# Kernel tuning notes

Measured on AMD Instinct MI355X. Metric: run time of the kernel, lower is better.

The kernel has to match this reference:

```python
import jax, jax.numpy as jnp
import numpy as np

B, S, D = 1, 1024, 1024
NH, NKV, HD = 16, 4, 64
E, K, HE = 64, 6, 512
EPS = 1e-5


def rmsnorm(x, w, eps=EPS):
    return w * (x * jax.lax.rsqrt(jnp.mean(x * x, axis=-1, keepdims=True) + eps))


def rope(x, cos, sin):
    # x: [b, s, h, hd]; cos/sin: [s, hd//2]; pairs are consecutive elements
    x2 = x.reshape(*x.shape[:-1], -1, 2)
    x0, x1 = x2[..., 0], x2[..., 1]
    c = cos[None, :, None, :]
    s = sin[None, :, None, :]
    o0 = x0 * c - x1 * s
    o1 = x0 * s + x1 * c
    return jnp.stack([o0, o1], axis=-1).reshape(x.shape)


def swiglu(x, w1, w3, w2):
    return (jax.nn.silu(x @ w1) * (x @ w3)) @ w2


def setup_inputs() -> dict:
    key = jax.random.key(0)
    ks = jax.random.split(key, 12)

    def w(k, shape, fan_in):
        return jax.random.normal(k, shape, jnp.float32) / np.sqrt(fan_in).astype(np.float32)

    # RoPE tables (theta = 10000), shape [S, HD//2]
    inv = 1.0 / (10000.0 ** (np.arange(0, HD, 2, dtype=np.float32) / HD))
    ang = np.arange(S, dtype=np.float32)[:, None] * inv[None, :]
    return {
        "x": jax.random.normal(ks[0], (B, S, D), jnp.float32),
        "freqs_cos": jnp.asarray(np.cos(ang), jnp.float32),
        "freqs_sin": jnp.asarray(np.sin(ang), jnp.float32),
        "attn_norm_w": jnp.ones((D,), jnp.float32),
        "ffn_norm_w": jnp.ones((D,), jnp.float32),
        "wq": w(ks[1], (D, NH * HD), D),
        "wk": w(ks[2], (D, NKV * HD), D),
        "wv": w(ks[3], (D, NKV * HD), D),
        "wo": w(ks[4], (NH * HD, D), NH * HD),
        "q_norm_w": jnp.ones((HD,), jnp.float32),
        "k_norm_w": jnp.ones((HD,), jnp.float32),
        "gate_w": w(ks[5], (D, E), D),
        "w1_e": w(ks[6], (E, D, HE), D),
        "w3_e": w(ks[7], (E, D, HE), D),
        "w2_e": w(ks[8], (E, HE, D), HE),
        "sw1": w(ks[9], (D, HE), D),
        "sw3": w(ks[10], (D, HE), D),
        "sw2": w(ks[11], (HE, D), HE),
    }


def reference(x, freqs_cos, freqs_sin, attn_norm_w, ffn_norm_w, wq, wk, wv, wo,
              q_norm_w, k_norm_w, gate_w, w1_e, w3_e, w2_e, sw1, sw3, sw2):
    b, s, d = x.shape
    # ---- attention (GQA + RoPE, causal) ----
    hx = rmsnorm(x, attn_norm_w)
    q = (hx @ wq).reshape(b, s, NH, HD)
    k = (hx @ wk).reshape(b, s, NKV, HD)
    v = (hx @ wv).reshape(b, s, NKV, HD)
    q = rmsnorm(q, q_norm_w)
    k = rmsnorm(k, k_norm_w)
    q = rope(q, freqs_cos, freqs_sin)
    k = rope(k, freqs_cos, freqs_sin)
    n_rep = NH // NKV
    k = jnp.repeat(k, n_rep, axis=2)  # [b,s,NH,HD]
    v = jnp.repeat(v, n_rep, axis=2)
    scores = jnp.einsum("bqhd,bkhd->bhqk", q, k) / jnp.float32(np.sqrt(HD))
    causal = jnp.tril(jnp.ones((s, s), bool))
    scores = jnp.where(causal[None, None], scores, jnp.finfo(scores.dtype).min)
    attn = jax.nn.softmax(scores, axis=-1)
    o = jnp.einsum("bhqk,bkhd->bqhd", attn, v).reshape(b, s, NH * HD) @ wo
    h = x + o

    # ---- MoE SwiGLU (top-k routing, renormalized) ----
    z = rmsnorm(h, ffn_norm_w).reshape(-1, d)  # [T, D]
    T = z.shape[0]
    probs = jax.nn.softmax(z @ gate_w, axis=-1)  # [T, E]
    topw, sel = jax.lax.top_k(probs, K)
    topw = topw / jnp.sum(topw, axis=-1, keepdims=True)
    # dense combine matrix C[t,e] = routing weight (0 if not selected)
    C = jnp.zeros((T, E), z.dtype).at[jnp.arange(T)[:, None], sel].add(topw)
    # expert SwiGLU, combine weights applied before the down-projection
    h1 = jnp.einsum("td,edh->teh", z, w1_e)
    h3 = jnp.einsum("td,edh->teh", z, w3_e)
    g = (jax.nn.silu(h1) * h3) * C[:, :, None]
    moe_out = jnp.einsum("teh,ehd->td", g, w2_e)
    shared = swiglu(z, sw1, sw3, sw2)
    return h + (moe_out + shared).reshape(b, s, d)
```

## Files before the change

### kernel.cpp

```cpp
#include <hip/hip_runtime.h>
#include <hip/hip_bf16.h>
#include <math.h>

#define D_MODEL 1024
#define SEQ     1024
#define NHEADS  16
#define NKVH    4
#define HDIM    64
#define NEXP    64
#define TOPK    6
#define HEXP    512
#define EPS     1e-5f
#define MAXTILES 120

typedef __attribute__((ext_vector_type(8))) short bf16x8;
typedef __attribute__((ext_vector_type(4))) float f32x4;

struct bfrag2 { bf16x8 hi, lo; };
struct f32x8r { float v[8]; };

__device__ __forceinline__ unsigned rne1(float a) {
  union { float f; unsigned u; } x; x.f = a;
  return (x.u + 0x7fffu + ((x.u >> 16) & 1u)) >> 16;
}
__device__ __forceinline__ float frombf(unsigned h) {
  union { float f; unsigned u; } x; x.u = h << 16; return x.f;
}
__device__ __forceinline__ void split_pack(float a, float b, unsigned& hi, unsigned& lo) {
  unsigned ha = rne1(a), hb = rne1(b);
  hi = ha | (hb << 16);
  lo = rne1(a - frombf(ha)) | (rne1(b - frombf(hb)) << 16);
}
__device__ __forceinline__ unsigned pk2bf(float a, float b) {
  return rne1(a) | (rne1(b) << 16);
}

__device__ __forceinline__ f32x4 mfma16(bf16x8 a, bf16x8 b, f32x4 c) {
  return __builtin_amdgcn_mfma_f32_16x16x32_bf16(a, b, c, 0, 0, 0);
}
__device__ __forceinline__ f32x4 mfma_sp(bf16x8 ah, bf16x8 al, const bfrag2& b, f32x4 c) {
  c = mfma16(ah, b.hi, c);
  c = mfma16(ah, b.lo, c);
  c = mfma16(al, b.hi, c);
  return c;
}

__device__ __forceinline__ f32x8r loadraw8(const float* __restrict__ p, int ld) {
  f32x8r r;
#pragma unroll
  for (int i = 0; i < 8; i++) r.v[i] = p[(size_t)ld * i];
  return r;
}
__device__ __forceinline__ bf16x8 cvt_bf(const f32x8r& f) {
  union { bf16x8 v; unsigned u[4]; } r;
  r.u[0] = pk2bf(f.v[0], f.v[1]); r.u[1] = pk2bf(f.v[2], f.v[3]);
  r.u[2] = pk2bf(f.v[4], f.v[5]); r.u[3] = pk2bf(f.v[6], f.v[7]);
  return r.v;
}
__device__ __forceinline__ bfrag2 cvt_bf2(const f32x8r& f) {
  union { bf16x8 v; unsigned u[4]; } H, L;
  split_pack(f.v[0], f.v[1], H.u[0], L.u[0]);
  split_pack(f.v[2], f.v[3], H.u[1], L.u[1]);
  split_pack(f.v[4], f.v[5], H.u[2], L.u[2]);
  split_pack(f.v[6], f.v[7], H.u[3], L.u[3]);
  bfrag2 r; r.hi = H.v; r.lo = L.v; return r;
}

__global__ __launch_bounds__(256) void rmsnorm_k(const float* __restrict__ x,
    const float* __restrict__ w, float* __restrict__ out, ushort* __restrict__ outb) {
  int t = blockIdx.x;
  const float4* xr = (const float4*)(x + (size_t)t * D_MODEL);
  float4 v = xr[threadIdx.x];
  float ss = v.x*v.x + v.y*v.y + v.z*v.z + v.w*v.w;
  for (int off = 32; off; off >>= 1) ss += __shfl_xor(ss, off);
  __shared__ float red[4];
  if ((threadIdx.x & 63) == 0) red[threadIdx.x >> 6] = ss;
  __syncthreads();
  float tot = red[0] + red[1] + red[2] + red[3];
  float inv = rsqrtf(tot * (1.f / D_MODEL) + EPS);
  float4 wv = ((const float4*)w)[threadIdx.x];
  float4 o;
  o.x = v.x * inv * wv.x; o.y = v.y * inv * wv.y;
  o.z = v.z * inv * wv.z; o.w = v.w * inv * wv.w;
  ((float4*)(out + (size_t)t * D_MODEL))[threadIdx.x] = o;
  if (outb) {
    uint2 b;
    b.x = pk2bf(o.x, o.y); b.y = pk2bf(o.z, o.w);
    *(uint2*)(outb + (size_t)t * D_MODEL + threadIdx.x * 4) = b;
  }
}

__global__ __launch_bounds__(256) void mfma_gemm_k(const float* __restrict__ A,
    const float* __restrict__ B, float* __restrict__ C, float* __restrict__ C2,
    const float* __restrict__ resid, int N, int K) {
  __shared__ short Ah[2][16][40];
  __shared__ short Al[2][16][40];
  int bm = blockIdx.y << 4, bn = blockIdx.x << 7;
  int tid = threadIdx.x, wv = tid >> 6, lane = tid & 63;
  int m_ = tid >> 4, k_ = (tid & 15) << 1;
  int arow = lane & 15, akb = (lane >> 4) << 3;
  int c0 = bn + wv * 32 + arow;
  const float* ar = A + (size_t)(bm + m_) * K + k_;
  {
    float2 a0 = *(const float2*)ar;
    unsigned hi, lo; split_pack(a0.x, a0.y, hi, lo);
    *(unsigned*)&Ah[0][m_][k_] = hi;
    *(unsigned*)&Al[0][m_][k_] = lo;
  }
  float2 aO = *(const float2*)(ar + 32);
  float2 aE;
  f32x8r bE0 = loadraw8(B + (size_t)akb * N + c0, N);
  f32x8r bE1 = loadraw8(B + (size_t)akb * N + c0 + 16, N);
  f32x8r bO0 = loadraw8(B + (size_t)(32 + akb) * N + c0, N);
  f32x8r bO1 = loadraw8(B + (size_t)(32 + akb) * N + c0 + 16, N);
  __syncthreads();
  f32x4 acc0 = {0.f,0.f,0.f,0.f}, acc1 = {0.f,0.f,0.f,0.f};
  for (int k0 = 0; k0 < K; k0 += 64) {
    {
      int kp = (k0 + 64 < K) ? k0 + 64 : 0;
      f32x8r n0 = loadraw8(B + (size_t)(kp + akb) * N + c0, N);
      f32x8r n1 = loadraw8(B + (size_t)(kp + akb) * N + c0 + 16, N);
      float2 an = *(const float2*)(ar + kp);
      bfrag2 f0 = cvt_bf2(bE0), f1 = cvt_bf2(bE1);
      bf16x8 ah = *(const bf16x8*)&Ah[0][arow][akb];
      bf16x8 al = *(const bf16x8*)&Al[0][arow][akb];
      acc0 = mfma_sp(ah, al, f0, acc0);
      acc1 = mfma_sp(ah, al, f1, acc1);
      unsigned hi, lo; split_pack(aO.x, aO.y, hi, lo);
      *(unsigned*)&Ah[1][m_][k_] = hi;
      *(unsigned*)&Al[1][m_][k_] = lo;
      __syncthreads();
      bE0 = n0; bE1 = n1; aE = an;
    }
    {
      int kp = (k0 + 96 < K) ? k0 + 96 : 0;
      f32x8r n0 = loadraw8(B + (size_t)(kp + akb) * N + c0, N);
      f32x8r n1 = loadraw8(B + (size_t)(kp + akb) * N + c0 + 16, N);
      float2 an = *(const float2*)(ar + kp);
      bfrag2 f0 = cvt_bf2(bO0), f1 = cvt_bf2(bO1);
      bf16x8 ah = *(const bf16x8*)&Ah[1][arow][akb];
      bf16x8 al = *(const bf16x8*)&Al[1][arow][akb];
      acc0 = mfma_sp(ah, al, f0, acc0);
      acc1 = mfma_sp(ah, al, f1, acc1);
      unsigned hi, lo; split_pack(aE.x, aE.y, hi, lo);
      *(unsigned*)&Ah[0][m_][k_] = hi;
      *(unsigned*)&Al[0][m_][k_] = lo;
      __syncthreads();
      bO0 = n0; bO1 = n1; aO = an;
    }
  }
  int r0 = (lane >> 4) << 2;
#pragma unroll
  for (int ri = 0; ri < 4; ri++) {
    int row = bm + r0 + ri;
    size_t o0 = (size_t)row * N + c0;
    float v0 = acc0[ri], v1 = acc1[ri];
    if (resid) { v0 += resid[o0]; v1 += resid[o0 + 16]; }
    C[o0] = v0; C[o0 + 16] = v1;
    if (C2) { C2[o0] = v0; C2[o0 + 16] = v1; }
  }
}

__global__ __launch_bounds__(64) void qknorm_rope_k(float* __restrict__ qb,
    float* __restrict__ kb, const float* __restrict__ qw, const float* __restrict__ kw,
    const float* __restrict__ fcos, const float* __restrict__ fsin) {
  int t = blockIdx.x, hid = blockIdx.y, lane = threadIdx.x;
  float* p; const float* w;
  if (hid < NHEADS) { p = qb + (size_t)t * (NHEADS*HDIM) + hid * HDIM; w = qw; }
  else              { p = kb + (size_t)t * (NKVH*HDIM) + (hid - NHEADS) * HDIM; w = kw; }
  float v = p[lane];
  float ss = v * v;
  for (int off = 32; off; off >>= 1) ss += __shfl_xor(ss, off);
  float vn = v * rsqrtf(ss * (1.f / HDIM) + EPS) * w[lane];
  int pi = lane >> 1;
  float c = fcos[t * (HDIM/2) + pi], s = fsin[t * (HDIM/2) + pi];
  float other = __shfl_xor(vn, 1);
  float o = (lane & 1) ? (other * s + vn * c) : (vn * c - other * s);
  p[lane] = o;
}

__global__ __launch_bounds__(256) void attn_mfma(const float* __restrict__ qb,
    const float* __restrict__ kb, const float* __restrict__ vb, float* __restrict__ ob) {
  int h = blockIdx.y;
  int qbase = blockIdx.x << 6;
  int kvh = h >> 2;
  int tid = threadIdx.x, wv = tid >> 6, lane = tid & 63;
  __shared__ short Kt[64][72];
  __shared__ short Vt[64][72];
  __shared__ short Pl[4][16][72];
  int arow = lane & 15;
  int akb = (lane >> 4) << 3;
  int kg = lane >> 4;
  int qrow_base = qbase + wv * 16;
  bf16x8 qf[2];
  {
    const float* qp = qb + (size_t)(qrow_base + arow) * (NHEADS*HDIM) + h * HDIM;
#pragma unroll
    for (int c = 0; c < 2; c++) {
      int d0 = akb + c * 32;
      union { bf16x8 v; unsigned u[4]; } r;
#pragma unroll
      for (int j = 0; j < 4; j++) r.u[j] = pk2bf(qp[d0 + 2*j], qp[d0 + 2*j + 1]);
      qf[c] = r.v;
    }
  }
  f32x4 accO[4];
  float m_[4], l_[4];
#pragma unroll
  for (int n = 0; n < 4; n++) { accO[n] = (f32x4){0.f,0.f,0.f,0.f}; m_[n] = -1e30f; l_[n] = 0.f; }
  int ntiles = (qbase >> 6) + 1;
  for (int ti = 0; ti < ntiles; ti++) {
    int ts = ti << 6;
#pragma unroll
    for (int i = 0; i < 16; i++) {
      int flat = tid + i * 256;
      int kk = flat >> 6, dd = flat & 63;
      size_t src = (size_t)(ts + kk) * (NKVH*HDIM) + kvh * HDIM + dd;
      Kt[kk][dd] = (short)rne1(kb[src]);
      Vt[dd][kk] = (short)rne1(vb[src]);
    }
    __syncthreads();
    f32x4 accS[4];
#pragma unroll
    for (int n = 0; n < 4; n++) accS[n] = (f32x4){0.f,0.f,0.f,0.f};
#pragma unroll
    for (int c = 0; c < 2; c++) {
#pragma unroll
      for (int n = 0; n < 4; n++) {
        bf16x8 bf = *(const bf16x8*)&Kt[n*16 + arow][c*32 + akb];
        accS[n] = mfma16(qf[c], bf, accS[n]);
      }
    }
#pragma unroll
    for (int ri = 0; ri < 4; ri++) {
      int qrow = qrow_base + kg*4 + ri;
      float mx = -1e30f;
#pragma unroll
      for (int n = 0; n < 4; n++) {
        int key = ts + n*16 + arow;
        float s = (key <= qrow) ? accS[n][ri] * 0.125f : -1e30f;
        accS[n][ri] = s;
        mx = fmaxf(mx, s);
      }
      for (int off = 1; off < 16; off <<= 1) mx = fmaxf(mx, __shfl_xor(mx, off));
      float mn = fmaxf(m_[ri], mx);
      float a = __expf(m_[ri] - mn);
      float sum = 0.f;
#pragma unroll
      for (int n = 0; n < 4; n++) {
        float p = __expf(accS[n][ri] - mn);
        accS[n][ri] = p;
        sum += p;
      }
      for (int off = 1; off < 16; off <<= 1) sum += __shfl_xor(sum, off);
      l_[ri] = l_[ri] * a + sum;
      m_[ri] = mn;
#pragma unroll
      for (int n = 0; n < 4; n++) accO[n][ri] *= a;
    }
#pragma unroll
    for (int ri = 0; ri < 4; ri++)
#pragma unroll
      for (int n = 0; n < 4; n++)
        Pl[wv][kg*4 + ri][n*16 + arow] = (short)rne1(accS[n][ri]);
#pragma unroll
    for (int c = 0; c < 2; c++) {
      bf16x8 pf = *(const bf16x8*)&Pl[wv][arow][c*32 + akb];
#pragma unroll
      for (int n = 0; n < 4; n++) {
        bf16x8 vf = *(const bf16x8*)&Vt[n*16 + arow][c*32 + akb];
        accO[n] = mfma16(pf, vf, accO[n]);
      }
    }
    __syncthreads();
  }
#pragma unroll
  for (int ri = 0; ri < 4; ri++) {
    int qrow = qrow_base + kg*4 + ri;
    float inv = 1.f / l_[ri];
#pragma unroll
    for (int n = 0; n < 4; n++)
      ob[(size_t)qrow * (NHEADS*HDIM) + h * HDIM + n*16 + arow] = accO[n][ri] * inv;
  }
}

__global__ __launch_bounds__(64) void gate_topk_k(const float* __restrict__ z,
    const float* __restrict__ gw, int* __restrict__ sel, float* __restrict__ topw,
    int* __restrict__ counts) {
  int t = blockIdx.x, lane = threadIdx.x;
  const float* zr = z + (size_t)t * D_MODEL;
  float acc = 0.f;
  for (int d = 0; d < D_MODEL; d += 4) {
    float4 zv = *(const float4*)(zr + d);
    acc += zv.x * gw[(size_t)(d + 0) * NEXP + lane];
    acc += zv.y * gw[(size_t)(d + 1) * NEXP + lane];
    acc += zv.z * gw[(size_t)(d + 2) * NEXP + lane];
    acc += zv.w * gw[(size_t)(d + 3) * NEXP + lane];
  }
  float m = acc;
  for (int off = 32; off; off >>= 1) m = fmaxf(m, __shfl_xor(m, off));
  float p = __expf(acc - m);
  float s = p;
  for (int off = 32; off; off >>= 1) s += __shfl_xor(s, off);
  p /= s;
  float rem = p, wsum = 0.f;
  float wvv[TOPK]; int wi[TOPK];
  for (int i = 0; i < TOPK; i++) {
    float v = rem; int idx = lane;
    for (int off = 32; off; off >>= 1) {
      float v2 = __shfl_xor(v, off);
      int i2 = __shfl_xor(idx, off);
      if (v2 > v || (v2 == v && i2 < idx)) { v = v2; idx = i2; }
    }
    wvv[i] = v; wi[i] = idx; wsum += v;
    if (lane == idx) rem = -1.f;
  }
  if (lane < TOPK) {
    sel[t * TOPK + lane] = wi[lane];
    topw[t * TOPK + lane] = wvv[lane] / wsum;
  }
  if (lane == 0)
    for (int i = 0; i < TOPK; i++) atomicAdd(&counts[wi[i]], 1);
}

__global__ void scan_k(const int* __restrict__ counts, int* __restrict__ offs,
                       int* __restrict__ cursor, int* __restrict__ tile2e,
                       int* __restrict__ tile2mt, int* __restrict__ ntiles) {
  int lane = threadIdx.x;
  int c = counts[lane];
  int x = c;
  for (int off = 1; off < 64; off <<= 1) {
    int y = __shfl_up(x, off);
    if (lane >= off) x += y;
  }
  offs[lane] = x - c;
  cursor[lane] = x - c;
  int nt = (c + 127) >> 7;
  int y = nt;
  for (int off = 1; off < 64; off <<= 1) {
    int t2 = __shfl_up(y, off);
    if (lane >= off) y += t2;
  }
  int tbase = y - nt;
  for (int i = 0; i < nt; i++) { tile2e[tbase + i] = lane; tile2mt[tbase + i] = i; }
  if (lane == 63) {
    for (int i = 0; i < 8; i++) { tile2e[y + i] = NEXP; tile2mt[y + i] = i; }
    ntiles[0] = y + 8;
  }
}

__global__ void scatter_k(const int* __restrict__ sel, const float* __restrict__ topw,
    int* __restrict__ cursor, int* __restrict__ tok, float* __restrict__ wt) {
  int t = blockIdx.x * 256 + threadIdx.x;
  if (t >= SEQ) return;
  for (int i = 0; i < TOPK; i++) {
    int e = sel[t * TOPK + i];
    int pos = atomicAdd(&cursor[e], 1);
    tok[pos] = t;
    wt[pos] = topw[t * TOPK + i];
  }
}

__global__ __launch_bounds__(256) void moe_up5(const ushort* __restrict__ zb,
    const float* __restrict__ w1, const float* __restrict__ w3, size_t wstride,
    const float* __restrict__ sw1, const float* __restrict__ sw3,
    ushort* __restrict__ g, ushort* __restrict__ sg,
    const int* __restrict__ tok_list, const float* __restrict__ wt_list,
    const int* __restrict__ counts, const int* __restrict__ offs,
    const int* __restrict__ tile2e, const int* __restrict__ tile2mt,
    const int* __restrict__ ntiles) {
  int gt = blockIdx.y;
  if (gt >= ntiles[0]) return;
  int e = tile2e[gt];
  int mt = tile2mt[gt] << 7;
  bool sh = (e == NEXP);
  int cnt = sh ? SEQ : counts[e];
  int off = sh ? 0 : offs[e];
  const float* w1p = sh ? sw1 : w1 + (size_t)e * wstride;
  const float* w3p = sh ? sw3 : w3 + (size_t)e * wstride;
  ushort* gout = sh ? sg : g;
  __shared__ ushort Ah[2][128][40];
  __shared__ int toks[128];
  int tid = threadIdx.x, wv = tid >> 6, lane = tid & 63;
  int arow = lane & 15, akb = (lane >> 4) << 3, kg = lane >> 4;
  int c0 = (blockIdx.x << 6) + wv * 16 + arow;
  if (tid < 128) {
    int r = mt + tid; if (r >= cnt) r = cnt - 1;
    toks[tid] = sh ? r : tok_list[off + r];
  }
  __syncthreads();
  int row0 = tid >> 2, q8 = (tid & 3) * 8;
  int row1 = row0 + 64;
  const ushort* zr0 = zb + (size_t)toks[row0] * D_MODEL + q8;
  const ushort* zr1 = zb + (size_t)toks[row1] * D_MODEL + q8;
  {
    uint4 t0 = *(const uint4*)zr0;
    uint4 t1 = *(const uint4*)zr1;
    *(uint4*)&Ah[0][row0][q8] = t0;
    *(uint4*)&Ah[0][row1][q8] = t1;
  }
  uint4 aO0 = *(const uint4*)(zr0 + 32);
  uint4 aO1 = *(const uint4*)(zr1 + 32);
  uint4 aE0, aE1;
  f32x8r bE1 = loadraw8(w1p + (size_t)akb * HEXP + c0, HEXP);
  f32x8r bE3 = loadraw8(w3p + (size_t)akb * HEXP + c0, HEXP);
  f32x8r bO1 = loadraw8(w1p + (size_t)(32 + akb) * HEXP + c0, HEXP);
  f32x8r bO3 = loadraw8(w3p + (size_t)(32 + akb) * HEXP + c0, HEXP);
  __syncthreads();
  f32x4 a1[8], a3[8];
#pragma unroll
  for (int f = 0; f < 8; f++) { a1[f] = (f32x4){0.f,0.f,0.f,0.f}; a3[f] = (f32x4){0.f,0.f,0.f,0.f}; }
  for (int k0 = 0; k0 < D_MODEL; k0 += 64) {
    {
      int kp = (k0 + 64 < D_MODEL) ? k0 + 64 : 0;
      f32x8r n1 = loadraw8(w1p + (size_t)(kp + akb) * HEXP + c0, HEXP);
      f32x8r n3 = loadraw8(w3p + (size_t)(kp + akb) * HEXP + c0, HEXP);
      uint4 an0 = *(const uint4*)(zr0 + kp);
      uint4 an1 = *(const uint4*)(zr1 + kp);
      bf16x8 b1 = cvt_bf(bE1), b3 = cvt_bf(bE3);
#pragma unroll
      for (int f = 0; f < 8; f++) {
        bf16x8 ah = *(const bf16x8*)&Ah[0][f*16 + arow][akb];
        a1[f] = mfma16(ah, b1, a1[f]);
        a3[f] = mfma16(ah, b3, a3[f]);
      }
      *(uint4*)&Ah[1][row0][q8] = aO0;
      *(uint4*)&Ah[1][row1][q8] = aO1;
      __syncthreads();
      bE1 = n1; bE3 = n3; aE0 = an0; aE1 = an1;
    }
    {
      int kp = (k0 + 96 < D_MODEL) ? k0 + 96 : 0;
      f32x8r n1 = loadraw8(w1p + (size_t)(kp + akb) * HEXP + c0, HEXP);
      f32x8r n3 = loadraw8(w3p + (size_t)(kp + akb) * HEXP + c0, HEXP);
      uint4 an0 = *(const uint4*)(zr0 + kp);
      uint4 an1 = *(const uint4*)(zr1 + kp);
      bf16x8 b1 = cvt_bf(bO1), b3 = cvt_bf(bO3);
#pragma unroll
      for (int f = 0; f < 8; f++) {
        bf16x8 ah = *(const bf16x8*)&Ah[1][f*16 + arow][akb];
        a1[f] = mfma16(ah, b1, a1[f]);
        a3[f] = mfma16(ah, b3, a3[f]);
      }
      *(uint4*)&Ah[0][row0][q8] = aE0;
      *(uint4*)&Ah[0][row1][q8] = aE1;
      __syncthreads();
      bO1 = n1; bO3 = n3; aO0 = an0; aO1 = an1;
    }
  }
#pragma unroll
  for (int f = 0; f < 8; f++)
#pragma unroll
    for (int ri = 0; ri < 4; ri++) {
      int r = mt + f*16 + kg*4 + ri;
      if (r < cnt) {
        float wt = sh ? 1.0f : wt_list[off + r];
        float h1 = a1[f][ri], h3 = a3[f][ri];
        float gv = h1 / (1.f + __expf(-h1)) * h3 * wt;
        gout[(size_t)(off + r) * HEXP + c0] = (ushort)rne1(gv);
      }
    }
}

__global__ __launch_bounds__(256) void moe_down5(const ushort* __restrict__ g,
    const ushort* __restrict__ sg, const float* __restrict__ w2, size_t wstride,
    const float* __restrict__ sw2, float* __restrict__ out,
    const int* __restrict__ tok_list, const int* __restrict__ counts,
    const int* __restrict__ offs, const int* __restrict__ tile2e,
    const int* __restrict__ tile2mt, const int* __restrict__ ntiles) {
  int gt = blockIdx.y;
  if (gt >= ntiles[0]) return;
  int e = tile2e[gt];
  int mt = tile2mt[gt] << 7;
  bool sh = (e == NEXP);
  int cnt = sh ? SEQ : counts[e];
  int off = sh ? 0 : offs[e];
  const float* w2p = sh ? sw2 : w2 + (size_t)e * wstride;
  const ushort* gin = sh ? sg : g;
  __shared__ ushort Ah[2][128][40];
  int tid = threadIdx.x, wv = tid >> 6, lane = tid & 63;
  int arow = lane & 15, akb = (lane >> 4) << 3, kg = lane >> 4;
  int c0 = (blockIdx.x << 7) + wv * 32 + arow;
  int row0 = tid >> 2, q8 = (tid & 3) * 8;
  int row1 = row0 + 64;
  int rr0 = mt + row0; if (rr0 >= cnt) rr0 = cnt - 1;
  int rr1 = mt + row1; if (rr1 >= cnt) rr1 = cnt - 1;
  const ushort* gr0 = gin + (size_t)(off + rr0) * HEXP + q8;
  const ushort* gr1 = gin + (size_t)(off + rr1) * HEXP + q8;
  {
    uint4 t0 = *(const uint4*)gr0;
    uint4 t1 = *(const uint4*)gr1;
    *(uint4*)&Ah[0][row0][q8] = t0;
    *(uint4*)&Ah[0][row1][q8] = t1;
  }
  uint4 aO0 = *(const uint4*)(gr0 + 32);
  uint4 aO1 = *(const uint4*)(gr1 + 32);
  uint4 aE0, aE1;
  f32x8r bEa = loadraw8(w2p + (size_t)akb * D_MODEL + c0, D_MODEL);
  f32x8r bEb = loadraw8(w2p + (size_t)akb * D_MODEL + c0 + 16, D_MODEL);
  f32x8r bOa = loadraw8(w2p + (size_t)(32 + akb) * D_MODEL + c0, D_MODEL);
  f32x8r bOb = loadraw8(w2p + (size_t)(32 + akb) * D_MODEL + c0 + 16, D_MODEL);
  __syncthreads();
  f32x4 ac0[8], ac1[8];
#pragma unroll
  for (int f = 0; f < 8; f++) { ac0[f] = (f32x4){0.f,0.f,0.f,0.f}; ac1[f] = (f32x4){0.f,0.f,0.f,0.f}; }
  for (int k0 = 0; k0 < HEXP; k0 += 64) {
    {
      int kp = (k0 + 64 < HEXP) ? k0 + 64 : 0;
      f32x8r na = loadraw8(w2p + (size_t)(kp + akb) * D_MODEL + c0, D_MODEL);
      f32x8r nb = loadraw8(w2p + (size_t)(kp + akb) * D_MODEL + c0 + 16, D_MODEL);
      uint4 an0 = *(const uint4*)(gr0 + kp);
      uint4 an1 = *(const uint4*)(gr1 + kp);
      bf16x8 b0 = cvt_bf(bEa), b1 = cvt_bf(bEb);
#pragma unroll
      for (int f = 0; f < 8; f++) {
        bf16x8 ah = *(const bf16x8*)&Ah[0][f*16 + arow][akb];
        ac0[f] = mfma16(ah, b0, ac0[f]);
        ac1[f] = mfma16(ah, b1, ac1[f]);
      }
      *(uint4*)&Ah[1][row0][q8] = aO0;
      *(uint4*)&Ah[1][row1][q8] = aO1;
      __syncthreads();
      bEa = na; bEb = nb; aE0 = an0; aE1 = an1;
    }
    {
      int kp = (k0 + 96 < HEXP) ? k0 + 96 : 0;
      f32x8r na = loadraw8(w2p + (size_t)(kp + akb) * D_MODEL + c0, D_MODEL);
      f32x8r nb = loadraw8(w2p + (size_t)(kp + akb) * D_MODEL + c0 + 16, D_MODEL);
      uint4 an0 = *(const uint4*)(gr0 + kp);
      uint4 an1 = *(const uint4*)(gr1 + kp);
      bf16x8 b0 = cvt_bf(bOa), b1 = cvt_bf(bOb);
#pragma unroll
      for (int f = 0; f < 8; f++) {
        bf16x8 ah = *(const bf16x8*)&Ah[1][f*16 + arow][akb];
        ac0[f] = mfma16(ah, b0, ac0[f]);
        ac1[f] = mfma16(ah, b1, ac1[f]);
      }
      *(uint4*)&Ah[0][row0][q8] = aE0;
      *(uint4*)&Ah[0][row1][q8] = aE1;
      __syncthreads();
      bOa = na; bOb = nb; aO0 = an0; aO1 = an1;
    }
  }
#pragma unroll
  for (int f = 0; f < 8; f++)
#pragma unroll
    for (int ri = 0; ri < 4; ri++) {
      int r = mt + f*16 + kg*4 + ri;
      if (r < cnt) {
        int tok = sh ? r : tok_list[off + r];
        float* op = out + (size_t)tok * D_MODEL + c0;
        atomicAdd(op, ac0[f][ri]);
        atomicAdd(op + 16, ac1[f][ri]);
      }
    }
}

extern "C" void kernel_launch(void* const* d_in, const int* in_sizes, int n_in,
                              void* d_out, int out_size, void* d_ws, size_t ws_size,
                              hipStream_t stream) {
  const float* x     = (const float*)d_in[0];
  const float* fcos  = (const float*)d_in[1];
  const float* fsin  = (const float*)d_in[2];
  const float* anw   = (const float*)d_in[3];
  const float* fnw   = (const float*)d_in[4];
  const float* wq    = (const float*)d_in[5];
  const float* wk    = (const float*)d_in[6];
  const float* wvv   = (const float*)d_in[7];
  const float* wo    = (const float*)d_in[8];
  const float* qnw   = (const float*)d_in[9];
  const float* knw   = (const float*)d_in[10];
  const float* gatew = (const float*)d_in[11];
  const float* w1e   = (const float*)d_in[12];
  const float* w3e   = (const float*)d_in[13];
  const float* w2e   = (const float*)d_in[14];
  const float* sw1   = (const float*)d_in[15];
  const float* sw3   = (const float*)d_in[16];
  const float* sw2   = (const float*)d_in[17];
  float* out = (float*)d_out;

  char* ws = (char*)d_ws;
  const size_t MB = 1ull << 20;
  float*  hx    = (float*)(ws);
  float*  h     = (float*)(ws + 4*MB);
  float*  z     = (float*)(ws + 8*MB);
  float*  qbuf  = (float*)(ws + 12*MB);
  float*  kbuf  = (float*)(ws + 16*MB);
  float*  vbuf  = (float*)(ws + 17*MB);
  ushort* zb    = (ushort*)(ws + 12*MB);
  ushort* gb    = (ushort*)(ws + 14*MB);
  ushort* s_gb  = (ushort*)(ws + 20*MB + 512*1024);
  char*   misc  = ws + 22*MB;
  int*   sel      = (int*)(misc);
  float* topw     = (float*)(misc + 24576);
  int*   counts   = (int*)(misc + 49152);
  int*   offs     = (int*)(misc + 49408);
  int*   cursor   = (int*)(misc + 49664);
  int*   ntiles   = (int*)(misc + 50432);
  int*   tile2e   = (int*)(misc + 50688);
  int*   tile2mt  = (int*)(misc + 51200);
  int*   tok_list = (int*)(misc + 51712);
  float* wt_list  = (float*)(misc + 76288);

  rmsnorm_k<<<SEQ, 256, 0, stream>>>(x, anw, hx, nullptr);
  mfma_gemm_k<<<dim3(8, 64), 256, 0, stream>>>(hx, wq, qbuf, nullptr, nullptr, 1024, 1024);
  mfma_gemm_k<<<dim3(2, 64), 256, 0, stream>>>(hx, wk, kbuf, nullptr, nullptr, 256, 1024);
  mfma_gemm_k<<<dim3(2, 64), 256, 0, stream>>>(hx, wvv, vbuf, nullptr, nullptr, 256, 1024);
  qknorm_rope_k<<<dim3(SEQ, NHEADS + NKVH), 64, 0, stream>>>(qbuf, kbuf, qnw, knw, fcos, fsin);
  attn_mfma<<<dim3(SEQ / 64, NHEADS), 256, 0, stream>>>(qbuf, kbuf, vbuf, hx);
  mfma_gemm_k<<<dim3(8, 64), 256, 0, stream>>>(hx, wo, h, out, x, 1024, 1024);
  rmsnorm_k<<<SEQ, 256, 0, stream>>>(h, fnw, z, zb);
  hipMemsetAsync(counts, 0, 256, stream);
  gate_topk_k<<<SEQ, 64, 0, stream>>>(z, gatew, sel, topw, counts);
  scan_k<<<1, 64, 0, stream>>>(counts, offs, cursor, tile2e, tile2mt, ntiles);
  scatter_k<<<SEQ / 256, 256, 0, stream>>>(sel, topw, cursor, tok_list, wt_list);
  moe_up5<<<dim3(HEXP / 64, MAXTILES), 256, 0, stream>>>(zb, w1e, w3e,
      (size_t)D_MODEL * HEXP, sw1, sw3, gb, s_gb, tok_list, wt_list,
      counts, offs, tile2e, tile2mt, ntiles);
  moe_down5<<<dim3(D_MODEL / 128, MAXTILES), 256, 0, stream>>>(gb, s_gb, w2e,
      (size_t)HEXP * D_MODEL, sw2, out, tok_list, counts, offs,
      tile2e, tile2mt, ntiles);
  (void)in_sizes; (void)n_in; (void)out_size; (void)ws_size;
}
```

Before: 413.3 us.

## Stage MoE expert weights through LDS with coalesced float4 loads and lighter barriers

The MoE up and down kernels now load weight tiles with coalesced float4 global loads. They convert them to bf16 and store them in a padded, double-buffered LDS tile, then build MFMA B fragments from LDS. This replaces the strided per-lane scalar gathers and register-resident conversion, and the K step drops from 64 to 32 with one barrier per step. __syncthreads in the dense GEMM and the new loops is replaced by an LDS-only waitcnt plus s_barrier, so outstanding global prefetches are not drained at each barrier. The cost is extra LDS traffic, possible bank conflicts in the per-element ushort fragment reads, and more LDS per block.

```diff
diff --git a/kernel.cpp b/kernel.cpp
--- a/kernel.cpp
+++ b/kernel.cpp
@@ -45,17 +45,16 @@
   return c;
 }
 
+__device__ __forceinline__ void barrier_nv() {
+  asm volatile("s_waitcnt lgkmcnt(0)" ::: "memory");
+  __builtin_amdgcn_s_barrier();
+}
+
 __device__ __forceinline__ f32x8r loadraw8(const float* __restrict__ p, int ld) {
   f32x8r r;
 #pragma unroll
   for (int i = 0; i < 8; i++) r.v[i] = p[(size_t)ld * i];
   return r;
-}
-__device__ __forceinline__ bf16x8 cvt_bf(const f32x8r& f) {
-  union { bf16x8 v; unsigned u[4]; } r;
-  r.u[0] = pk2bf(f.v[0], f.v[1]); r.u[1] = pk2bf(f.v[2], f.v[3]);
-  r.u[2] = pk2bf(f.v[4], f.v[5]); r.u[3] = pk2bf(f.v[6], f.v[7]);
-  return r.v;
 }
 __device__ __forceinline__ bfrag2 cvt_bf2(const f32x8r& f) {
   union { bf16x8 v; unsigned u[4]; } H, L;
@@ -64,6 +63,14 @@
   split_pack(f.v[4], f.v[5], H.u[2], L.u[2]);
   split_pack(f.v[6], f.v[7], H.u[3], L.u[3]);
   bfrag2 r; r.hi = H.v; r.lo = L.v; return r;
+}
+
+template<int RL>
+__device__ __forceinline__ bf16x8 bfrag_lds(const ushort* __restrict__ B, int akb, int c) {
+  union { bf16x8 v; ushort s[8]; } r;
+#pragma unroll
+  for (int j = 0; j < 8; j++) r.s[j] = B[(akb + j) * RL + c];
+  return r.v;
 }
 
 __global__ __launch_bounds__(256) void rmsnorm_k(const float* __restrict__ x,
@@ -129,7 +136,7 @@
       unsigned hi, lo; split_pack(aO.x, aO.y, hi, lo);
       *(unsigned*)&Ah[1][m_][k_] = hi;
       *(unsigned*)&Al[1][m_][k_] = lo;
-      __syncthreads();
+      barrier_nv();
       bE0 = n0; bE1 = n1; aE = an;
     }
     {
@@ -145,7 +152,7 @@
       unsigned hi, lo; split_pack(aE.x, aE.y, hi, lo);
       *(unsigned*)&Ah[0][m_][k_] = hi;
       *(unsigned*)&Al[0][m_][k_] = lo;
-      __syncthreads();
+      barrier_nv();
       bO0 = n0; bO1 = n1; aO = an;
     }
   }
@@ -361,7 +368,7 @@
   }
 }
 
-__global__ __launch_bounds__(256) void moe_up5(const ushort* __restrict__ zb,
+__global__ __launch_bounds__(256) void moe_up6(const ushort* __restrict__ zb,
     const float* __restrict__ w1, const float* __restrict__ w3, size_t wstride,
     const float* __restrict__ sw1, const float* __restrict__ sw3,
     ushort* __restrict__ g, ushort* __restrict__ sg,
@@ -376,77 +383,71 @@
   bool sh = (e == NEXP);
   int cnt = sh ? SEQ : counts[e];
   int off = sh ? 0 : offs[e];
-  const float* w1p = sh ? sw1 : w1 + (size_t)e * wstride;
-  const float* w3p = sh ? sw3 : w3 + (size_t)e * wstride;
+  const float* w1p = (sh ? sw1 : w1 + (size_t)e * wstride) + (blockIdx.x << 6);
+  const float* w3p = (sh ? sw3 : w3 + (size_t)e * wstride) + (blockIdx.x << 6);
   ushort* gout = sh ? sg : g;
   __shared__ ushort Ah[2][128][40];
+  __shared__ ushort Bs[2][2][32][74];
   __shared__ int toks[128];
   int tid = threadIdx.x, wv = tid >> 6, lane = tid & 63;
   int arow = lane & 15, akb = (lane >> 4) << 3, kg = lane >> 4;
-  int c0 = (blockIdx.x << 6) + wv * 16 + arow;
+  int c0l = wv * 16 + arow;
+  int c0 = (blockIdx.x << 6) + c0l;
   if (tid < 128) {
     int r = mt + tid; if (r >= cnt) r = cnt - 1;
     toks[tid] = sh ? r : tok_list[off + r];
   }
   __syncthreads();
-  int row0 = tid >> 2, q8 = (tid & 3) * 8;
-  int row1 = row0 + 64;
+  int row0 = tid >> 2, q8 = (tid & 3) << 3, row1 = row0 + 64;
   const ushort* zr0 = zb + (size_t)toks[row0] * D_MODEL + q8;
   const ushort* zr1 = zb + (size_t)toks[row1] * D_MODEL + q8;
-  {
-    uint4 t0 = *(const uint4*)zr0;
-    uint4 t1 = *(const uint4*)zr1;
-    *(uint4*)&Ah[0][row0][q8] = t0;
-    *(uint4*)&Ah[0][row1][q8] = t1;
-  }
-  uint4 aO0 = *(const uint4*)(zr0 + 32);
-  uint4 aO1 = *(const uint4*)(zr1 + 32);
-  uint4 aE0, aE1;
-  f32x8r bE1 = loadraw8(w1p + (size_t)akb * HEXP + c0, HEXP);
-  f32x8r bE3 = loadraw8(w3p + (size_t)akb * HEXP + c0, HEXP);
-  f32x8r bO1 = loadraw8(w1p + (size_t)(32 + akb) * HEXP + c0, HEXP);
-  f32x8r bO3 = loadraw8(w3p + (size_t)(32 + akb) * HEXP + c0, HEXP);
-  __syncthreads();
+  int kB = tid >> 4, cB = (tid & 15) << 2;
+  const float* w1q = w1p + (size_t)kB * HEXP + cB;
+  const float* w3q = w3p + (size_t)kB * HEXP + cB;
+  uint4  ra0 = *(const uint4*)zr0;
+  uint4  ra1 = *(const uint4*)zr1;
+  float4 rb1a = *(const float4*)w1q;
+  float4 rb1b = *(const float4*)(w1q + 16 * HEXP);
+  float4 rb3a = *(const float4*)w3q;
+  float4 rb3b = *(const float4*)(w3q + 16 * HEXP);
   f32x4 a1[8], a3[8];
 #pragma unroll
   for (int f = 0; f < 8; f++) { a1[f] = (f32x4){0.f,0.f,0.f,0.f}; a3[f] = (f32x4){0.f,0.f,0.f,0.f}; }
-  for (int k0 = 0; k0 < D_MODEL; k0 += 64) {
+  int cur = 0;
+  for (int k0 = 0; k0 < D_MODEL; k0 += 32) {
+    int kp = (k0 + 32 < D_MODEL) ? k0 + 32 : 0;
+    uint4  na0 = *(const uint4*)(zr0 + kp);
+    uint4  na1 = *(const uint4*)(zr1 + kp);
+    const float* w1n = w1q + (size_t)kp * HEXP;
+    const float* w3n = w3q + (size_t)kp * HEXP;
+    float4 nb1a = *(const float4*)w1n;
+    float4 nb1b = *(const float4*)(w1n + 16 * HEXP);
+    float4 nb3a = *(const float4*)w3n;
+    float4 nb3b = *(const float4*)(w3n + 16 * HEXP);
+    *(uint4*)&Ah[cur][row0][q8] = ra0;
+    *(uint4*)&Ah[cur][row1][q8] = ra1;
     {
-      int kp = (k0 + 64 < D_MODEL) ? k0 + 64 : 0;
-      f32x8r n1 = loadraw8(w1p + (size_t)(kp + akb) * HEXP + c0, HEXP);
-      f32x8r n3 = loadraw8(w3p + (size_t)(kp + akb) * HEXP + c0, HEXP);
-      uint4 an0 = *(const uint4*)(zr0 + kp);
-      uint4 an1 = *(const uint4*)(zr1 + kp);
-      bf16x8 b1 = cvt_bf(bE1), b3 = cvt_bf(bE3);
-#pragma unroll
-      for (int f = 0; f < 8; f++) {
-        bf16x8 ah = *(const bf16x8*)&Ah[0][f*16 + arow][akb];
-        a1[f] = mfma16(ah, b1, a1[f]);
-        a3[f] = mfma16(ah, b3, a3[f]);
-      }
-      *(uint4*)&Ah[1][row0][q8] = aO0;
-      *(uint4*)&Ah[1][row1][q8] = aO1;
-      __syncthreads();
-      bE1 = n1; bE3 = n3; aE0 = an0; aE1 = an1;
-    }
-    {
-      int kp = (k0 + 96 < D_MODEL) ? k0 + 96 : 0;
-      f32x8r n1 = loadraw8(w1p + (size_t)(kp + akb) * HEXP + c0, HEXP);
-      f32x8r n3 = loadraw8(w3p + (size_t)(kp + akb) * HEXP + c0, HEXP);
-      uint4 an0 = *(const uint4*)(zr0 + kp);
-      uint4 an1 = *(const uint4*)(zr1 + kp);
-      bf16x8 b1 = cvt_bf(bO1), b3 = cvt_bf(bO3);
-#pragma unroll
-      for (int f = 0; f < 8; f++) {
-        bf16x8 ah = *(const bf16x8*)&Ah[1][f*16 + arow][akb];
-        a1[f] = mfma16(ah, b1, a1[f]);
-        a3[f] = mfma16(ah, b3, a3[f]);
-      }
-      *(uint4*)&Ah[0][row0][q8] = aE0;
-      *(uint4*)&Ah[0][row1][q8] = aE1;
-      __syncthreads();
-      bO1 = n1; bO3 = n3; aO0 = an0; aO1 = an1;
-    }
+      unsigned* p = (unsigned*)&Bs[cur][0][kB][cB];
+      p[0] = pk2bf(rb1a.x, rb1a.y); p[1] = pk2bf(rb1a.z, rb1a.w);
+      unsigned* p2 = (unsigned*)&Bs[cur][0][kB + 16][cB];
+      p2[0] = pk2bf(rb1b.x, rb1b.y); p2[1] = pk2bf(rb1b.z, rb1b.w);
+      unsigned* p3 = (unsigned*)&Bs[cur][1][kB][cB];
+      p3[0] = pk2bf(rb3a.x, rb3a.y); p3[1] = pk2bf(rb3a.z, rb3a.w);
+      unsigned* p4 = (unsigned*)&Bs[cur][1][kB + 16][cB];
+      p4[0] = pk2bf(rb3b.x, rb3b.y); p4[1] = pk2bf(rb3b.z, rb3b.w);
+    }
+    barrier_nv();
+    bf16x8 f1 = bfrag_lds<74>(&Bs[cur][0][0][0], akb, c0l);
+    bf16x8 f3 = bfrag_lds<74>(&Bs[cur][1][0][0], akb, c0l);
+#pragma unroll
+    for (int f = 0; f < 8; f++) {
+      bf16x8 ah = *(const bf16x8*)&Ah[cur][f*16 + arow][akb];
+      a1[f] = mfma16(ah, f1, a1[f]);
+      a3[f] = mfma16(ah, f3, a3[f]);
+    }
+    ra0 = na0; ra1 = na1;
+    rb1a = nb1a; rb1b = nb1b; rb3a = nb3a; rb3b = nb3b;
+    cur ^= 1;
   }
 #pragma unroll
   for (int f = 0; f < 8; f++)
@@ -462,7 +463,7 @@
     }
 }
 
-__global__ __launch_bounds__(256) void moe_down5(const ushort* __restrict__ g,
+__global__ __launch_bounds__(256) void moe_down6(const ushort* __restrict__ g,
     const ushort* __restrict__ sg, const float* __restrict__ w2, size_t wstride,
     const float* __restrict__ sw2, float* __restrict__ out,
     const int* __restrict__ tok_list, const int* __restrict__ counts,
@@ -475,72 +476,61 @@
   bool sh = (e == NEXP);
   int cnt = sh ? SEQ : counts[e];
   int off = sh ? 0 : offs[e];
-  const float* w2p = sh ? sw2 : w2 + (size_t)e * wstride;
+  const float* w2p = (sh ? sw2 : w2 + (size_t)e * wstride) + (blockIdx.x << 7);
   const ushort* gin = sh ? sg : g;
   __shared__ ushort Ah[2][128][40];
+  __shared__ ushort Bs[2][32][138];
   int tid = threadIdx.x, wv = tid >> 6, lane = tid & 63;
   int arow = lane & 15, akb = (lane >> 4) << 3, kg = lane >> 4;
-  int c0 = (blockIdx.x << 7) + wv * 32 + arow;
-  int row0 = tid >> 2, q8 = (tid & 3) * 8;
-  int row1 = row0 + 64;
+  int c0l = wv * 32 + arow;
+  int c0 = (blockIdx.x << 7) + c0l;
+  int row0 = tid >> 2, q8 = (tid & 3) << 3, row1 = row0 + 64;
   int rr0 = mt + row0; if (rr0 >= cnt) rr0 = cnt - 1;
   int rr1 = mt + row1; if (rr1 >= cnt) rr1 = cnt - 1;
   const ushort* gr0 = gin + (size_t)(off + rr0) * HEXP + q8;
   const ushort* gr1 = gin + (size_t)(off + rr1) * HEXP + q8;
-  {
-    uint4 t0 = *(const uint4*)gr0;
-    uint4 t1 = *(const uint4*)gr1;
-    *(uint4*)&Ah[0][row0][q8] = t0;
-    *(uint4*)&Ah[0][row1][q8] = t1;
-  }
-  uint4 aO0 = *(const uint4*)(gr0 + 32);
-  uint4 aO1 = *(const uint4*)(gr1 + 32);
-  uint4 aE0, aE1;
-  f32x8r bEa = loadraw8(w2p + (size_t)akb * D_MODEL + c0, D_MODEL);
-  f32x8r bEb = loadraw8(w2p + (size_t)akb * D_MODEL + c0 + 16, D_MODEL);
-  f32x8r bOa = loadraw8(w2p + (size_t)(32 + akb) * D_MODEL + c0, D_MODEL);
-  f32x8r bOb = loadraw8(w2p + (size_t)(32 + akb) * D_MODEL + c0 + 16, D_MODEL);
-  __syncthreads();
+  int kB = tid >> 3, cB = (tid & 7) << 4;
+  const float* w2q = w2p + (size_t)kB * D_MODEL + cB;
+  uint4  ra0 = *(const uint4*)gr0;
+  uint4  ra1 = *(const uint4*)gr1;
+  float4 rb0 = *(const float4*)(w2q);
+  float4 rb1 = *(const float4*)(w2q + 4);
+  float4 rb2 = *(const float4*)(w2q + 8);
+  float4 rb3 = *(const float4*)(w2q + 12);
   f32x4 ac0[8], ac1[8];
 #pragma unroll
   for (int f = 0; f < 8; f++) { ac0[f] = (f32x4){0.f,0.f,0.f,0.f}; ac1[f] = (f32x4){0.f,0.f,0.f,0.f}; }
-  for (int k0 = 0; k0 < HEXP; k0 += 64) {
+  int cur = 0;
+  for (int k0 = 0; k0 < HEXP; k0 += 32) {
+    int kp = (k0 + 32 < HEXP) ? k0 + 32 : 0;
+    uint4  na0 = *(const uint4*)(gr0 + kp);
+    uint4  na1 = *(const uint4*)(gr1 + kp);
+    const float* wn = w2q + (size_t)kp * D_MODEL;
+    float4 nb0 = *(const float4*)(wn);
+    float4 nb1 = *(const float4*)(wn + 4);
+    float4 nb2 = *(const float4*)(wn + 8);
+    float4 nb3 = *(const float4*)(wn + 12);
+    *(uint4*)&Ah[cur][row0][q8] = ra0;
+    *(uint4*)&Ah[cur][row1][q8] = ra1;
     {
-      int kp = (k0 + 64 < HEXP) ? k0 + 64 : 0;
-      f32x8r na = loadraw8(w2p + (size_t)(kp + akb) * D_MODEL + c0, D_MODEL);
-      f32x8r nb = loadraw8(w2p + (size_t)(kp + akb) * D_MODEL + c0 + 16, D_MODEL);
-      uint4 an0 = *(const uint4*)(gr0 + kp);
-      uint4 an1 = *(const uint4*)(gr1 + kp);
-      bf16x8 b0 = cvt_bf(bEa), b1 = cvt_bf(bEb);
-#pragma unroll
-      for (int f = 0; f < 8; f++) {
-        bf16x8 ah = *(const bf16x8*)&Ah[0][f*16 + arow][akb];
-        ac0[f] = mfma16(ah, b0, ac0[f]);
-        ac1[f] = mfma16(ah, b1, ac1[f]);
-      }
-      *(uint4*)&Ah[1][row0][q8] = aO0;
-      *(uint4*)&Ah[1][row1][q8] = aO1;
-      __syncthreads();
-      bEa = na; bEb = nb; aE0 = an0; aE1 = an1;
-    }
-    {
-      int kp = (k0 + 96 < HEXP) ? k0 + 96 : 0;
-      f32x8r na = loadraw8(w2p + (size_t)(kp + akb) * D_MODEL + c0, D_MODEL);
-      f32x8r nb = loadraw8(w2p + (size_t)(kp + akb) * D_MODEL + c0 + 16, D_MODEL);
-      uint4 an0 = *(const uint4*)(gr0 + kp);
-      uint4 an1 = *(const uint4*)(gr1 + kp);
-      bf16x8 b0 = cvt_bf(bOa), b1 = cvt_bf(bOb);
-#pragma unroll
-      for (int f = 0; f < 8; f++) {
-        bf16x8 ah = *(const bf16x8*)&Ah[1][f*16 + arow][akb];
-        ac0[f] = mfma16(ah, b0, ac0[f]);
-        ac1[f] = mfma16(ah, b1, ac1[f]);
-      }
-      *(uint4*)&Ah[0][row0][q8] = aE0;
-      *(uint4*)&Ah[0][row1][q8] = aE1;
-      __syncthreads();
-      bOa = na; bOb = nb; aO0 = an0; aO1 = an1;
-    }
+      unsigned* p = (unsigned*)&Bs[cur][kB][cB];
+      p[0] = pk2bf(rb0.x, rb0.y); p[1] = pk2bf(rb0.z, rb0.w);
+      p[2] = pk2bf(rb1.x, rb1.y); p[3] = pk2bf(rb1.z, rb1.w);
+      p[4] = pk2bf(rb2.x, rb2.y); p[5] = pk2bf(rb2.z, rb2.w);
+      p[6] = pk2bf(rb3.x, rb3.y); p[7] = pk2bf(rb3.z, rb3.w);
+    }
+    barrier_nv();
+    bf16x8 f0 = bfrag_lds<138>(&Bs[cur][0][0], akb, c0l);
+    bf16x8 f1 = bfrag_lds<138>(&Bs[cur][0][0], akb, c0l + 16);
+#pragma unroll
+    for (int f = 0; f < 8; f++) {
+      bf16x8 ah = *(const bf16x8*)&Ah[cur][f*16 + arow][akb];
+      ac0[f] = mfma16(ah, f0, ac0[f]);
+      ac1[f] = mfma16(ah, f1, ac1[f]);
+    }
+    ra0 = na0; ra1 = na1;
+    rb0 = nb0; rb1 = nb1; rb2 = nb2; rb3 = nb3;
+    cur ^= 1;
   }
 #pragma unroll
   for (int f = 0; f < 8; f++)
@@ -614,10 +604,10 @@
   gate_topk_k<<<SEQ, 64, 0, stream>>>(z, gatew, sel, topw, counts);
   scan_k<<<1, 64, 0, stream>>>(counts, offs, cursor, tile2e, tile2mt, ntiles);
   scatter_k<<<SEQ / 256, 256, 0, stream>>>(sel, topw, cursor, tok_list, wt_list);
-  moe_up5<<<dim3(HEXP / 64, MAXTILES), 256, 0, stream>>>(zb, w1e, w3e,
+  moe_up6<<<dim3(HEXP / 64, MAXTILES), 256, 0, stream>>>(zb, w1e, w3e,
       (size_t)D_MODEL * HEXP, sw1, sw3, gb, s_gb, tok_list, wt_list,
       counts, offs, tile2e, tile2mt, ntiles);
-  moe_down5<<<dim3(D_MODEL / 128, MAXTILES), 256, 0, stream>>>(gb, s_gb, w2e,
+  moe_down6<<<dim3(D_MODEL / 128, MAXTILES), 256, 0, stream>>>(gb, s_gb, w2e,
       (size_t)HEXP * D_MODEL, sw2, out, tok_list, counts, offs,
       tile2e, tile2mt, ntiles);
   (void)in_sizes; (void)n_in; (void)out_size; (void)ws_size;
```

After: 382.1 us. 1.08x faster.
